# Performance work log

Measured on AMD Instinct MI355X. Metric: run time of the kernel, lower is better.

## Reference

```python
import jax, jax.numpy as jnp
import numpy as np

B, T, D_MODEL, H, RPR_K = 2, 2048, 1024, 16, 8
DK = D_MODEL // H  # 64
NUM_RPR = 2 * RPR_K + 1


def setup_inputs() -> dict:
    key = jax.random.key(0)
    ks = jax.random.split(key, 16)
    s = 0.02
    inp = {
        "query": jax.random.normal(ks[0], (B, T, D_MODEL), jnp.float32),
        "key": jax.random.normal(ks[1], (B, T, D_MODEL), jnp.float32),
        "value": jax.random.normal(ks[2], (B, T, D_MODEL), jnp.float32),
        "mask": jnp.ones((B, 1, 1, T), dtype=bool),
        "w_q": jax.random.normal(ks[3], (D_MODEL, H * DK), jnp.float32) * s,
        "b_q": jnp.zeros((H * DK,), jnp.float32),
        "w_k": jax.random.normal(ks[4], (D_MODEL, H * DK), jnp.float32) * s,
        "b_k": jnp.zeros((H * DK,), jnp.float32),
        "w_v": jax.random.normal(ks[5], (D_MODEL, H * DK), jnp.float32) * s,
        "b_v": jnp.zeros((H * DK,), jnp.float32),
        "w_o": jax.random.normal(ks[6], (H * DK, D_MODEL), jnp.float32) * s,
        "b_o": jnp.zeros((D_MODEL,), jnp.float32),
        "rpr_key_table": jax.random.normal(ks[7], (NUM_RPR, DK), jnp.float32),
        "rpr_value_table": jax.random.normal(ks[8], (NUM_RPR, DK), jnp.float32),
    }
    return inp


def _rel_edges(seq_len):
    # edges[i, j] = clamp(j - i + rpr_k, 0, 2*rpr_k)  -> [T, T] int32
    seq = jnp.arange(seq_len)
    edges = seq[None, :] - seq[:, None] + RPR_K
    return jnp.clip(edges, 0, 2 * RPR_K)


def reference(query, key, value, mask, w_q, b_q, w_k, b_k, w_v, b_v,
              w_o, b_o, rpr_key_table, rpr_value_table):
    Bsz, Tlen, _ = query.shape
    edges = _rel_edges(Tlen)                       # [T, T]
    ek = rpr_key_table[edges]                      # [T, T, DK]
    ev = rpr_value_table[edges]                    # [T, T, DK]

    def proj(x, w, b):
        return (x @ w + b).reshape(Bsz, Tlen, H, DK).transpose(0, 2, 1, 3)  # [B,H,T,DK]

    q = proj(query, w_q, b_q)
    k = proj(key, w_k, b_k)
    v = proj(value, w_v, b_v)

    scores_qk = jnp.einsum('bhtd,bhsd->bhts', q, k)
    scores_qek = jnp.einsum('bhtd,tsd->bhts', q, ek)
    scores = (scores_qk + scores_qek) / jnp.sqrt(jnp.float32(DK))
    scores = jnp.where(mask, scores, jnp.float32(-1e9))
    a = jax.nn.softmax(scores, axis=-1)            # [B,H,T,T]

    upd = jnp.einsum('bhts,bhsd->bhtd', a, v)
    upd_e = jnp.einsum('bhts,tsd->bhtd', a, ev)
    x = (upd + upd_e).transpose(0, 2, 1, 3).reshape(Bsz, Tlen, H * DK)
    return x @ w_o + b_o
```

## Files before the change

### kernel.cpp

```cpp
#include <hip/hip_runtime.h>
#include <stdint.h>


typedef unsigned short u16;
typedef __attribute__((ext_vector_type(4))) float f32x4;
typedef __attribute__((ext_vector_type(16))) float f32x16;
typedef __attribute__((ext_vector_type(4))) int   i32x4;
typedef __attribute__((ext_vector_type(8))) __bf16 bh8;

#define T_LEN 2048
#define NHEAD 16
#define NR    17

#define SCALE_LOG2 0.18033688011112042f
#define CLAMP_LOG2 86.56170245333781f

__device__ __forceinline__ float bf2f(u16 x) {
  unsigned u = ((unsigned)x) << 16;
  return __builtin_bit_cast(float, u);
}
__device__ __forceinline__ u16 f2bf(float f) {
  unsigned u = __builtin_bit_cast(unsigned, f);
  u = u + 0x7fffu + ((u >> 16) & 1u);
  return (u16)(u >> 16);
}
__device__ __forceinline__ f32x4 zero4() { f32x4 z = {0.f, 0.f, 0.f, 0.f}; return z; }
__device__ __forceinline__ f32x16 zero16() {
  f32x16 z = {0.f, 0.f, 0.f, 0.f, 0.f, 0.f, 0.f, 0.f,
              0.f, 0.f, 0.f, 0.f, 0.f, 0.f, 0.f, 0.f};
  return z;
}

__device__ __forceinline__ f32x4 mfma16(bh8 a, bh8 b, f32x4 c) {
  return __builtin_amdgcn_mfma_f32_16x16x32_bf16(a, b, c, 0, 0, 0);
}
__device__ __forceinline__ f32x16 mfma32(bh8 a, bh8 b, f32x16 c) {
  return __builtin_amdgcn_mfma_f32_32x32x16_bf16(a, b, c, 0, 0, 0);
}

__device__ __forceinline__ unsigned cvtpk(float a, float b) {
  unsigned r;
  asm("v_cvt_pk_bf16_f32 %0, %1, %2" : "=v"(r) : "v"(a), "v"(b));
  return r;
}

__device__ __forceinline__ void bar_sync() {
  __builtin_amdgcn_sched_barrier(0);
  asm volatile("s_waitcnt lgkmcnt(0)" ::: "memory");
  __builtin_amdgcn_s_barrier();
  __builtin_amdgcn_sched_barrier(0);
}

__device__ __forceinline__ void wait_vm0() {
  __builtin_amdgcn_sched_barrier(0);
  asm volatile("s_waitcnt vmcnt(0)" ::: "memory");
  __builtin_amdgcn_sched_barrier(0);
}

__device__ __forceinline__ void async16(const u16* g, u16* l) {
  __builtin_amdgcn_global_load_lds(
      (const __attribute__((address_space(1))) void*)g,
      (__attribute__((address_space(3))) void*)l, 16, 0, 0);
}

__device__ __forceinline__ bh8 ldfrag(const u16* base, int row, int qc) {
  const i32x4 v = *(const i32x4*)(base + row * 64 + ((qc ^ (row & 7)) << 3));
  return __builtin_bit_cast(bh8, v);
}

__global__ __launch_bounds__(256) void prep_kernel(
    const float* __restrict__ xq, const float* __restrict__ xk,
    const float* __restrict__ xv, const float* __restrict__ w0,
    const float* __restrict__ w1, const float* __restrict__ w2,
    const float* __restrict__ w3, u16* __restrict__ oq, u16* __restrict__ ok,
    u16* __restrict__ ov, u16* __restrict__ t0, u16* __restrict__ t1,
    u16* __restrict__ t2, u16* __restrict__ t3) {
  __shared__ u16 tile[32][33];
  const int z = blockIdx.z;
  if (z < 3) {
    const float* S = (z == 0) ? xq : (z == 1) ? xk : xv;
    u16* D = (z == 0) ? oq : (z == 1) ? ok : ov;
    const size_t i = ((size_t)blockIdx.x * 256 + threadIdx.x) * 8;
    const f32x4 v0 = *(const f32x4*)(S + i);
    const f32x4 v1 = *(const f32x4*)(S + i + 4);
    u16 o[8];
#pragma unroll
    for (int j = 0; j < 4; ++j) {
      o[j] = f2bf(v0[j]);
      o[4 + j] = f2bf(v1[j]);
    }
    i32x4 w;
    __builtin_memcpy(&w, o, 16);
    *(i32x4*)(D + i) = w;
  } else {
    if (blockIdx.x >= 1024) return;
    const float* S = (z == 3) ? w0 : (z == 4) ? w1 : (z == 5) ? w2 : w3;
    u16* D = (z == 3) ? t0 : (z == 4) ? t1 : (z == 5) ? t2 : t3;
    const int tx = threadIdx.x & 31, ty = threadIdx.x >> 5;
    const int bx = blockIdx.x & 31, by = blockIdx.x >> 5;
#pragma unroll
    for (int i = 0; i < 4; ++i) {
      const int y = by * 32 + ty + i * 8;
      tile[ty + i * 8][tx] = f2bf(S[(size_t)y * 1024 + bx * 32 + tx]);
    }
    __syncthreads();
#pragma unroll
    for (int i = 0; i < 4; ++i) {
      const int y = bx * 32 + ty + i * 8;
      D[(size_t)y * 1024 + by * 32 + tx] = tile[tx][ty + i * 8];
    }
  }
}

__device__ __forceinline__ void gemm_body(const u16* __restrict__ A,
                                          const u16* __restrict__ Bm,
                                          const float* __restrict__ bias,
                                          void* __restrict__ out, int mode,
                                          int bm, int bn) {
  __shared__ __align__(16) u16 As[2][128 * 32];
  __shared__ __align__(16) u16 Bs[2][128 * 32];
  const int tid = threadIdx.x;
  const int wv = tid >> 6;
  const int ln = tid & 63;
  const int quad = ln >> 4, l15 = ln & 15;
  const int wr = wv >> 1, wc = wv & 1;

  f32x4 acc[4][4];
#pragma unroll
  for (int i = 0; i < 4; ++i)
#pragma unroll
    for (int j = 0; j < 4; ++j) acc[i][j] = zero4();

  const int c0 = tid, c1 = tid + 256;
  const size_t aoff0 = (size_t)(bm * 128 + (c0 >> 2)) * 1024 + (c0 & 3) * 8;
  const size_t aoff1 = (size_t)(bm * 128 + (c1 >> 2)) * 1024 + (c1 & 3) * 8;
  const size_t boff0 = (size_t)(bn * 128 + (c0 >> 2)) * 1024 + (c0 & 3) * 8;
  const size_t boff1 = (size_t)(bn * 128 + (c1 >> 2)) * 1024 + (c1 & 3) * 8;

  u16* ad0[2] = {&As[0][(wv * 64) * 8], &As[1][(wv * 64) * 8]};
  u16* ad1[2] = {&As[0][(256 + wv * 64) * 8], &As[1][(256 + wv * 64) * 8]};
  u16* bd0[2] = {&Bs[0][(wv * 64) * 8], &Bs[1][(wv * 64) * 8]};
  u16* bd1[2] = {&Bs[0][(256 + wv * 64) * 8], &Bs[1][(256 + wv * 64) * 8]};

  async16(A + aoff0, ad0[0]);
  async16(A + aoff1, ad1[0]);
  async16(Bm + boff0, bd0[0]);
  async16(Bm + boff1, bd1[0]);
  __syncthreads();

  for (int kt = 0; kt < 32; ++kt) {
    const int cur = kt & 1, nxt = cur ^ 1;
    if (kt < 31) {
      const int ko = (kt + 1) * 32;
      async16(A + aoff0 + ko, ad0[nxt]);
      async16(A + aoff1 + ko, ad1[nxt]);
      async16(Bm + boff0 + ko, bd0[nxt]);
      async16(Bm + boff1 + ko, bd1[nxt]);
    }

    bh8 af[4], bf[4];
#pragma unroll
    for (int mi = 0; mi < 4; ++mi)
      af[mi] = __builtin_bit_cast(
          bh8,
          *(const i32x4*)&As[cur][(wr * 64 + mi * 16 + l15) * 32 + quad * 8]);
#pragma unroll
    for (int ni = 0; ni < 4; ++ni)
      bf[ni] = __builtin_bit_cast(
          bh8,
          *(const i32x4*)&Bs[cur][(wc * 64 + ni * 16 + l15) * 32 + quad * 8]);
#pragma unroll
    for (int mi = 0; mi < 4; ++mi)
#pragma unroll
      for (int ni = 0; ni < 4; ++ni)
        acc[mi][ni] = mfma16(af[mi], bf[ni], acc[mi][ni]);

    __syncthreads();
  }

#pragma unroll
  for (int mi = 0; mi < 4; ++mi) {
    const int row0 = bm * 128 + wr * 64 + mi * 16 + quad * 4;
#pragma unroll
    for (int ni = 0; ni < 4; ++ni) {
      const int col = bn * 128 + wc * 64 + ni * 16 + l15;
      const float bcol = (mode == 3) ? 0.f : bias[col];
#pragma unroll
      for (int reg = 0; reg < 4; ++reg) {
        const int r = row0 + reg;
        const float v = acc[mi][ni][reg] + ((mode == 3) ? bias[r] : bcol);
        if (mode == 1) {
          const int bb = r >> 11, t = r & 2047;
          const int h = col >> 6, d = col & 63;
          ((u16*)out)[(((size_t)bb * NHEAD + h) * T_LEN + (size_t)t) * 64 + d] =
              f2bf(v);
        } else {
          const int h = r >> 6, d = r & 63;
          const int bb = col >> 11, t = col & 2047;
          ((u16*)out)[(((size_t)bb * NHEAD + h) * 64 + (size_t)d) * T_LEN + t] =
              f2bf(v);
        }
      }
    }
  }
}

__global__ __launch_bounds__(256) void gemm_qkv_kernel(
    const u16* __restrict__ xq, const u16* __restrict__ xk,
    const u16* __restrict__ xv, const u16* __restrict__ wtq,
    const u16* __restrict__ wtk, const u16* __restrict__ wtv,
    const float* __restrict__ bq, const float* __restrict__ bk,
    const float* __restrict__ bv, u16* __restrict__ oq, u16* __restrict__ ok,
    u16* __restrict__ ovt) {
  const int z = blockIdx.z;
  if (z == 0)
    gemm_body(xq, wtq, bq, oq, 1, blockIdx.x, blockIdx.y);
  else if (z == 1)
    gemm_body(xk, wtk, bk, ok, 1, blockIdx.x, blockIdx.y);
  else
    gemm_body(wtv, xv, bv, ovt, 3, blockIdx.y, blockIdx.x);
}

__global__ __launch_bounds__(256) void gemm_o_kernel(const u16* __restrict__ A,
                                                     const u16* __restrict__ Bm,
                                                     const float* __restrict__ bias,
                                                     float* __restrict__ out) {
  __shared__ __align__(16) u16 As[2][64 * 32];
  __shared__ __align__(16) u16 Bs[2][128 * 32];
  const int tid = threadIdx.x;
  const int wv = tid >> 6;
  const int ln = tid & 63;
  const int quad = ln >> 4, l15 = ln & 15;
  const int wr = wv >> 1, wc = wv & 1;
  const int bm = blockIdx.x, bn = blockIdx.y;

  f32x4 acc[2][4];
#pragma unroll
  for (int i = 0; i < 2; ++i)
#pragma unroll
    for (int j = 0; j < 4; ++j) acc[i][j] = zero4();

  const int c0 = tid, c1 = tid + 256;
  const size_t aoff0 = (size_t)(bm * 64 + (c0 >> 2)) * 1024 + (c0 & 3) * 8;
  const size_t boff0 = (size_t)(bn * 128 + (c0 >> 2)) * 1024 + (c0 & 3) * 8;
  const size_t boff1 = (size_t)(bn * 128 + (c1 >> 2)) * 1024 + (c1 & 3) * 8;

  u16* ad0[2] = {&As[0][(wv * 64) * 8], &As[1][(wv * 64) * 8]};
  u16* bd0[2] = {&Bs[0][(wv * 64) * 8], &Bs[1][(wv * 64) * 8]};
  u16* bd1[2] = {&Bs[0][(256 + wv * 64) * 8], &Bs[1][(256 + wv * 64) * 8]};

  async16(A + aoff0, ad0[0]);
  async16(Bm + boff0, bd0[0]);
  async16(Bm + boff1, bd1[0]);
  __syncthreads();

  for (int kt = 0; kt < 32; ++kt) {
    const int cur = kt & 1, nxt = cur ^ 1;
    if (kt < 31) {
      const int ko = (kt + 1) * 32;
      async16(A + aoff0 + ko, ad0[nxt]);
      async16(Bm + boff0 + ko, bd0[nxt]);
      async16(Bm + boff1 + ko, bd1[nxt]);
    }

    bh8 af[2], bf[4];
#pragma unroll
    for (int mi = 0; mi < 2; ++mi)
      af[mi] = __builtin_bit_cast(
          bh8,
          *(const i32x4*)&As[cur][(wr * 32 + mi * 16 + l15) * 32 + quad * 8]);
#pragma unroll
    for (int ni = 0; ni < 4; ++ni)
      bf[ni] = __builtin_bit_cast(
          bh8,
          *(const i32x4*)&Bs[cur][(wc * 64 + ni * 16 + l15) * 32 + quad * 8]);
#pragma unroll
    for (int mi = 0; mi < 2; ++mi)
#pragma unroll
      for (int ni = 0; ni < 4; ++ni)
        acc[mi][ni] = mfma16(af[mi], bf[ni], acc[mi][ni]);

    __syncthreads();
  }

#pragma unroll
  for (int mi = 0; mi < 2; ++mi) {
    const int row0 = bm * 64 + wr * 32 + mi * 16 + quad * 4;
#pragma unroll
    for (int ni = 0; ni < 4; ++ni) {
      const int col = bn * 128 + wc * 64 + ni * 16 + l15;
      const float bcol = bias[col];
#pragma unroll
      for (int reg = 0; reg < 4; ++reg)
        out[(size_t)(row0 + reg) * 1024 + col] = acc[mi][ni][reg] + bcol;
    }
  }
}

__global__ __launch_bounds__(256, 3) void attn_kernel(
    const u16* __restrict__ Qw, const u16* __restrict__ Kw,
    const u16* __restrict__ Vtw, const float* __restrict__ rkt,
    const float* __restrict__ rvt, u16* __restrict__ U) {
  __shared__ __align__(16) u16 smu[16384];
  __shared__ float smf[4480];
  u16* const Qs = smu;
  float* const qes = smf;
  float* const aw15 = smf + 2176;
  float* const lp = smf + 4096;
  float* const aw0 = smf + 4224;
  float* const aw16 = smf + 4352;
  float* const rvs = (float*)smu;

  const int tid = threadIdx.x;
  const int wv = tid >> 6, ln = tid & 63;
  const int l31 = ln & 31, hi = ln >> 5;
  const int wg = blockIdx.x;
  const int xcd = wg & 7;
  const int slot = wg >> 3;
  const int qt = slot & 15;
  const int bh = xcd * 4 + (slot >> 4);
  const size_t hb = (size_t)bh * (T_LEN * 64);
  const int t0 = qt * 128 + wv * 32;
  const int tl = wv * 32 + l31;

  const int r8 = ln >> 3, c8 = ln & 7;
  const int kgp = c8 ^ (r8 & 7);
  const u16* ksrc0 = Kw + hb + (size_t)(wv * 16 + r8) * 64 + kgp * 8;
  const u16* ksrc1 = Kw + hb + (size_t)(wv * 16 + 8 + r8) * 64 + kgp * 8;
  const u16* vsrc0 = Vtw + hb + (size_t)(wv * 16 + r8) * T_LEN + kgp * 8;
  const u16* vsrc1 = Vtw + hb + (size_t)(wv * 16 + 8 + r8) * T_LEN + kgp * 8;
  u16* const ldsK0 = smu + (wv * 16) * 64;
  u16* const ldsK1 = smu + (wv * 16 + 8) * 64;
  u16* const ldsV0 = smu + 8192 + (wv * 16) * 64;
  u16* const ldsV1 = smu + 8192 + (wv * 16 + 8) * 64;

  {
    const u16* qsrc = Qw + hb + (size_t)(qt * 128 + wv * 32 + r8) * 64 + kgp * 8;
#pragma unroll
    for (int a = 0; a < 4; ++a)
      async16(qsrc + (size_t)(a * 8) * 64, Qs + (wv * 32 + a * 8) * 64);
  }
  wait_vm0();
  bar_sync();

  for (int i = tid; i < 128 * NR; i += 256) {
    const int row = i / NR, r = i - row * NR;
    float s = 0.f;
#pragma unroll
    for (int c = 0; c < 8; ++c) {
      const i32x4 qv = *(const i32x4*)&Qs[row * 64 + ((c ^ (row & 7)) << 3)];
      const u16* qq = (const u16*)&qv;
#pragma unroll
      for (int j = 0; j < 8; ++j) s += bf2f(qq[j]) * rkt[r * 64 + c * 8 + j];
    }
    qes[i] = s;
  }
  for (int i = tid; i < 128 * 15; i += 256) aw15[i] = 0.f;
  bar_sync();

  const float qb0 = qes[tl * NR + 0] * SCALE_LOG2;
  const float qb16 = qes[tl * NR + 16] * SCALE_LOG2;
  bh8 qf[4];
#pragma unroll
  for (int kb = 0; kb < 4; ++kb) qf[kb] = ldfrag(Qs, tl, kb * 2 + hi);
  bar_sync();

  async16(ksrc0, ldsK0);
  async16(ksrc1, ldsK1);
  async16(vsrc0, ldsV0);
  async16(vsrc1, ldsV1);
  wait_vm0();
  bar_sync();

  float l_l = 0.f, s0_l = 0.f, s16_l = 0.f;
  f32x16 oacc[2] = {zero16(), zero16()};

  for (int st = 0; st < 32; ++st) {
    const int cur = st & 1;
    const u16* Kc = smu + cur * 4096;
    const u16* Vc = smu + 8192 + cur * 4096;
    if (st < 31) {
      const int nxt = cur ^ 1;
      async16(ksrc0 + (size_t)(st + 1) * 4096, ldsK0 + nxt * 4096);
      async16(ksrc1 + (size_t)(st + 1) * 4096, ldsK1 + nxt * 4096);
      async16(vsrc0 + (size_t)(st + 1) * 64, ldsV0 + nxt * 4096);
      async16(vsrc1 + (size_t)(st + 1) * 64, ldsV1 + nxt * 4096);
    }
    __builtin_amdgcn_s_setprio(1);

#pragma unroll
    for (int sb = 0; sb < 2; ++sb) {
      f32x16 sacc = zero16();
#pragma unroll
      for (int kb = 0; kb < 4; ++kb) {
        const bh8 kf = ldfrag(Kc, sb * 32 + l31, kb * 2 + hi);
        sacc = mfma32(kf, qf[kb], sacc);
      }

      const int sbase = st * 64 + sb * 32;
      float p[16];
      if (sbase + 39 <= t0) {
        float ts = 0.f;
#pragma unroll
        for (int r = 0; r < 16; ++r) {
          const float x = fminf(sacc[r] * SCALE_LOG2 + qb0, CLAMP_LOG2);
          const float pv = __builtin_amdgcn_exp2f(x);
          p[r] = pv;
          ts += pv;
        }
        l_l += ts;
        s0_l += ts;
      } else if (sbase >= t0 + 39) {
        float ts = 0.f;
#pragma unroll
        for (int r = 0; r < 16; ++r) {
          const float x = fminf(sacc[r] * SCALE_LOG2 + qb16, CLAMP_LOG2);
          const float pv = __builtin_amdgcn_exp2f(x);
          p[r] = pv;
          ts += pv;
        }
        l_l += ts;
        s16_l += ts;
      } else {
        const int base = sbase + 4 * hi - (t0 + l31) + 8;
#pragma unroll
        for (int r = 0; r < 16; ++r) {
          int rel = base + (r & 3) + 8 * (r >> 2);
          rel = rel < 0 ? 0 : (rel > 16 ? 16 : rel);
          const float x = fminf((sacc[r] + qes[tl * NR + rel]) * SCALE_LOG2,
                                CLAMP_LOG2);
          const float pv = __builtin_amdgcn_exp2f(x);
          p[r] = pv;
          l_l += pv;
          if (rel == 0)
            s0_l += pv;
          else if (rel == 16)
            s16_l += pv;
          else
            atomicAdd(&aw15[tl * 15 + rel - 1], pv);
        }
      }

#pragma unroll
      for (int h = 0; h < 2; ++h) {
        unsigned wa = cvtpk(p[8 * h + 0], p[8 * h + 1]);
        unsigned wb = cvtpk(p[8 * h + 2], p[8 * h + 3]);
        unsigned wc = cvtpk(p[8 * h + 4], p[8 * h + 5]);
        unsigned wd = cvtpk(p[8 * h + 6], p[8 * h + 7]);
        asm("v_permlane32_swap_b32 %0, %1" : "+v"(wa), "+v"(wc));
        asm("v_permlane32_swap_b32 %0, %1" : "+v"(wb), "+v"(wd));
        const i32x4 fr = {(int)wa, (int)wb, (int)wc, (int)wd};
        const bh8 pa = __builtin_bit_cast(bh8, fr);
        const int ks = sb * 2 + h;
#pragma unroll
        for (int db = 0; db < 2; ++db) {
          const bh8 vf = ldfrag(Vc, db * 32 + l31, ks * 2 + hi);
          oacc[db] = mfma32(pa, vf, oacc[db]);
        }
      }
    }
    __builtin_amdgcn_s_setprio(0);

    wait_vm0();
    bar_sync();
  }

  l_l += __shfl_xor(l_l, 32);
  s0_l += __shfl_xor(s0_l, 32);
  s16_l += __shfl_xor(s16_l, 32);
  if (ln < 32) {
    lp[tl] = l_l;
    aw0[tl] = s0_l;
    aw16[tl] = s16_l;
  }
  for (int i = tid; i < NR * 64; i += 256) rvs[i] = rvt[i];
  __syncthreads();

  const int bb = bh >> 4, hh = bh & 15;
#pragma unroll
  for (int r = 0; r < 16; ++r) {
    const int srow = (r & 3) + 8 * (r >> 2) + 4 * hi;
    const int trow = wv * 32 + srow;
    const float linv = 1.f / lp[trow];
    float e0 = aw0[trow] * rvs[l31] + aw16[trow] * rvs[16 * 64 + l31];
    float e1 = aw0[trow] * rvs[32 + l31] + aw16[trow] * rvs[16 * 64 + 32 + l31];
#pragma unroll
    for (int rr = 1; rr < 16; ++rr) {
      const float awv = aw15[trow * 15 + rr - 1];
      e0 += awv * rvs[rr * 64 + l31];
      e1 += awv * rvs[rr * 64 + 32 + l31];
    }
    const int tg = qt * 128 + trow;
    const size_t ubase = ((size_t)bb * T_LEN + tg) * 1024 + hh * 64;
    U[ubase + l31] = f2bf((oacc[0][r] + e0) * linv);
    U[ubase + 32 + l31] = f2bf((oacc[1][r] + e1) * linv);
  }
}

extern "C" void kernel_launch(void* const* d_in, const int* in_sizes, int n_in,
                              void* d_out, int out_size, void* d_ws,
                              size_t ws_size, hipStream_t stream) {
  const float* query = (const float*)d_in[0];
  const float* key = (const float*)d_in[1];
  const float* value = (const float*)d_in[2];
  const float* w_q = (const float*)d_in[4];
  const float* b_q = (const float*)d_in[5];
  const float* w_k = (const float*)d_in[6];
  const float* b_k = (const float*)d_in[7];
  const float* w_v = (const float*)d_in[8];
  const float* b_v = (const float*)d_in[9];
  const float* w_o = (const float*)d_in[10];
  const float* b_o = (const float*)d_in[11];
  const float* rkt = (const float*)d_in[12];
  const float* rvt = (const float*)d_in[13];

  char* ws = (char*)d_ws;
  const size_t MB2 = 1u << 21, MB8 = 1u << 23;
  u16* wtq = (u16*)(ws + 0 * MB2);
  u16* wtk = (u16*)(ws + 1 * MB2);
  u16* wtv = (u16*)(ws + 2 * MB2);
  u16* wto = (u16*)(ws + 3 * MB2);
  u16* Xq = (u16*)(ws + 4 * MB2 + 0 * MB8);
  u16* Xk = (u16*)(ws + 4 * MB2 + 1 * MB8);
  u16* Xv = (u16*)(ws + 4 * MB2 + 2 * MB8);
  u16* Qw = (u16*)(ws + 4 * MB2 + 3 * MB8);
  u16* Kw = (u16*)(ws + 4 * MB2 + 4 * MB8);
  u16* Vtw = (u16*)(ws + 4 * MB2 + 5 * MB8);
  u16* Uw = (u16*)(ws + 4 * MB2 + 6 * MB8);

  prep_kernel<<<dim3(2048, 1, 7), 256, 0, stream>>>(
      query, key, value, w_q, w_k, w_v, w_o, Xq, Xk, Xv, wtq, wtk, wtv, wto);
  gemm_qkv_kernel<<<dim3(32, 8, 3), 256, 0, stream>>>(
      Xq, Xk, Xv, wtq, wtk, wtv, b_q, b_k, b_v, Qw, Kw, Vtw);
  attn_kernel<<<dim3(512), 256, 0, stream>>>(Qw, Kw, Vtw, rkt, rvt, Uw);
  gemm_o_kernel<<<dim3(64, 8), 256, 0, stream>>>(Uw, wto, b_o, (float*)d_out);
}
```

Measured before the change: 271.1 us.

## Split attention KV range across two workgroups and combine partials in new kernel

Each (batch, head, query-tile) attention job is split into two workgroups. One handles key tiles near the diagonal, where the relative-position bias varies. The other handles the far tiles, where the bias is the constant index-16 term. Partial outputs and softmax sums go to float workspace buffers, and a new combine kernel merges them, adds the rpr-value contribution and writes bf16 U in a blocked layout that the output GEMM reads. It also folds the softmax scale into the Q projection and drops the exp clamp and max-free rescaling. This doubles the workgroup count for better occupancy and load balance, at the cost of an extra kernel launch, extra fp32 traffic, and a possible overflow risk without the clamp.

```diff
diff --git a/kernel.cpp b/kernel.cpp
--- a/kernel.cpp
+++ b/kernel.cpp
@@ -13,7 +13,12 @@
 #define NR    17
 
 #define SCALE_LOG2 0.18033688011112042f
-#define CLAMP_LOG2 86.56170245333781f
+
+#define AW15_OFF 0
+#define LA_OFF   1048576
+#define A0_OFF   1114112
+#define A16_OFF  1179648
+#define LB_OFF   1245184
 
 __device__ __forceinline__ float bf2f(u16 x) {
   unsigned u = ((unsigned)x) << 16;
@@ -116,7 +121,7 @@
                                           const u16* __restrict__ Bm,
                                           const float* __restrict__ bias,
                                           void* __restrict__ out, int mode,
-                                          int bm, int bn) {
+                                          int bm, int bn, float oscale) {
   __shared__ __align__(16) u16 As[2][128 * 32];
   __shared__ __align__(16) u16 Bs[2][128 * 32];
   const int tid = threadIdx.x;
@@ -193,7 +198,7 @@
           const int bb = r >> 11, t = r & 2047;
           const int h = col >> 6, d = col & 63;
           ((u16*)out)[(((size_t)bb * NHEAD + h) * T_LEN + (size_t)t) * 64 + d] =
-              f2bf(v);
+              f2bf(v * oscale);
         } else {
           const int h = r >> 6, d = r & 63;
           const int bb = col >> 11, t = col & 2047;
@@ -214,14 +219,14 @@
     u16* __restrict__ ovt) {
   const int z = blockIdx.z;
   if (z == 0)
-    gemm_body(xq, wtq, bq, oq, 1, blockIdx.x, blockIdx.y);
+    gemm_body(xq, wtq, bq, oq, 1, blockIdx.x, blockIdx.y, SCALE_LOG2);
   else if (z == 1)
-    gemm_body(xk, wtk, bk, ok, 1, blockIdx.x, blockIdx.y);
+    gemm_body(xk, wtk, bk, ok, 1, blockIdx.x, blockIdx.y, 1.f);
   else
-    gemm_body(wtv, xv, bv, ovt, 3, blockIdx.y, blockIdx.x);
-}
-
-__global__ __launch_bounds__(256) void gemm_o_kernel(const u16* __restrict__ A,
+    gemm_body(wtv, xv, bv, ovt, 3, blockIdx.y, blockIdx.x, 1.f);
+}
+
+__global__ __launch_bounds__(256) void gemm_o_kernel(const u16* __restrict__ Ublk,
                                                      const u16* __restrict__ Bm,
                                                      const float* __restrict__ bias,
                                                      float* __restrict__ out) {
@@ -241,7 +246,9 @@
     for (int j = 0; j < 4; ++j) acc[i][j] = zero4();
 
   const int c0 = tid, c1 = tid + 256;
-  const size_t aoff0 = (size_t)(bm * 64 + (c0 >> 2)) * 1024 + (c0 & 3) * 8;
+  const int rA = bm * 64 + (c0 >> 2);
+  const int tA = rA & 2047, bbA = rA >> 11;
+  const size_t abase = (size_t)(tA >> 7);
   const size_t boff0 = (size_t)(bn * 128 + (c0 >> 2)) * 1024 + (c0 & 3) * 8;
   const size_t boff1 = (size_t)(bn * 128 + (c1 >> 2)) * 1024 + (c1 & 3) * 8;
 
@@ -249,7 +256,14 @@
   u16* bd0[2] = {&Bs[0][(wv * 64) * 8], &Bs[1][(wv * 64) * 8]};
   u16* bd1[2] = {&Bs[0][(256 + wv * 64) * 8], &Bs[1][(256 + wv * 64) * 8]};
 
-  async16(A + aoff0, ad0[0]);
+  auto aoff = [&](int kt) -> size_t {
+    const int c = kt * 32 + (c0 & 3) * 8;
+    const int h = c >> 6, d = c & 63;
+    const size_t idx = (size_t)(bbA * 16 + h) * 16 + abase;
+    return idx * 16384 + (size_t)(tA & 127) * 64 + d;
+  };
+
+  async16(Ublk + aoff(0), ad0[0]);
   async16(Bm + boff0, bd0[0]);
   async16(Bm + boff1, bd1[0]);
   __syncthreads();
@@ -258,7 +272,7 @@
     const int cur = kt & 1, nxt = cur ^ 1;
     if (kt < 31) {
       const int ko = (kt + 1) * 32;
-      async16(A + aoff0 + ko, ad0[nxt]);
+      async16(Ublk + aoff(kt + 1), ad0[nxt]);
       async16(Bm + boff0 + ko, bd0[nxt]);
       async16(Bm + boff1 + ko, bd1[nxt]);
     }
@@ -300,28 +314,43 @@
 __global__ __launch_bounds__(256, 3) void attn_kernel(
     const u16* __restrict__ Qw, const u16* __restrict__ Kw,
     const u16* __restrict__ Vtw, const float* __restrict__ rkt,
-    const float* __restrict__ rvt, u16* __restrict__ U) {
+    float* __restrict__ Oa, float* __restrict__ ObLo, float* __restrict__ ObHi,
+    float* __restrict__ awb) {
   __shared__ __align__(16) u16 smu[16384];
-  __shared__ float smf[4480];
+  __shared__ float smf[4096];
   u16* const Qs = smu;
   float* const qes = smf;
   float* const aw15 = smf + 2176;
-  float* const lp = smf + 4096;
-  float* const aw0 = smf + 4224;
-  float* const aw16 = smf + 4352;
-  float* const rvs = (float*)smu;
 
   const int tid = threadIdx.x;
   const int wv = tid >> 6, ln = tid & 63;
   const int l31 = ln & 31, hi = ln >> 5;
   const int wg = blockIdx.x;
   const int xcd = wg & 7;
-  const int slot = wg >> 3;
-  const int qt = slot & 15;
-  const int bh = xcd * 4 + (slot >> 4);
+  const int rest = wg >> 3;
+  const int sh = rest >> 6;
+  const int sub = rest & 63;
+  const int qt = sub & 15;
+  const int bh = xcd * 4 + (sub >> 4);
+  const int idx = bh * 16 + qt;
   const size_t hb = (size_t)bh * (T_LEN * 64);
   const int t0 = qt * 128 + wv * 32;
   const int tl = wv * 32 + l31;
+
+  const int cut = (2 * qt + 3 > 32) ? 32 : (2 * qt + 3);
+  const int stBeg = sh ? cut : 0;
+  const int stEnd = sh ? 32 : cut;
+
+  float* const opart = (sh == 0)
+                           ? (Oa + (size_t)idx * 8192)
+                           : (idx < 256 ? ObLo + (size_t)idx * 8192
+                                        : ObHi + (size_t)(idx - 256) * 8192);
+
+  if (stBeg >= stEnd) {
+    for (int i = tid; i < 8192; i += 256) opart[i] = 0.f;
+    if (tid < 128) awb[LB_OFF + idx * 128 + tid] = 0.f;
+    return;
+  }
 
   const int r8 = ln >> 3, c8 = ln & 7;
   const int kgp = c8 ^ (r8 & 7);
@@ -343,43 +372,61 @@
   wait_vm0();
   bar_sync();
 
-  for (int i = tid; i < 128 * NR; i += 256) {
-    const int row = i / NR, r = i - row * NR;
-    float s = 0.f;
-#pragma unroll
-    for (int c = 0; c < 8; ++c) {
-      const i32x4 qv = *(const i32x4*)&Qs[row * 64 + ((c ^ (row & 7)) << 3)];
-      const u16* qq = (const u16*)&qv;
-#pragma unroll
-      for (int j = 0; j < 8; ++j) s += bf2f(qq[j]) * rkt[r * 64 + c * 8 + j];
-    }
-    qes[i] = s;
-  }
-  for (int i = tid; i < 128 * 15; i += 256) aw15[i] = 0.f;
+  if (sh == 0) {
+    for (int i = tid; i < 128 * NR; i += 256) {
+      const int row = i / NR, r = i - row * NR;
+      float s = 0.f;
+#pragma unroll
+      for (int c = 0; c < 8; ++c) {
+        const i32x4 qv = *(const i32x4*)&Qs[row * 64 + ((c ^ (row & 7)) << 3)];
+        const u16* qq = (const u16*)&qv;
+#pragma unroll
+        for (int j = 0; j < 8; ++j) s += bf2f(qq[j]) * rkt[r * 64 + c * 8 + j];
+      }
+      qes[i] = s;
+    }
+    for (int i = tid; i < 128 * 15; i += 256) aw15[i] = 0.f;
+  } else {
+    for (int row = tid; row < 128; row += 256) {
+      float s = 0.f;
+#pragma unroll
+      for (int c = 0; c < 8; ++c) {
+        const i32x4 qv = *(const i32x4*)&Qs[row * 64 + ((c ^ (row & 7)) << 3)];
+        const u16* qq = (const u16*)&qv;
+#pragma unroll
+        for (int j = 0; j < 8; ++j)
+          s += bf2f(qq[j]) * rkt[16 * 64 + c * 8 + j];
+      }
+      qes[row * NR + 16] = s;
+    }
+  }
   bar_sync();
 
-  const float qb0 = qes[tl * NR + 0] * SCALE_LOG2;
-  const float qb16 = qes[tl * NR + 16] * SCALE_LOG2;
+  const float qb0 = (sh == 0) ? qes[tl * NR + 0] : 0.f;
+  const float qb16 = qes[tl * NR + 16];
   bh8 qf[4];
 #pragma unroll
   for (int kb = 0; kb < 4; ++kb) qf[kb] = ldfrag(Qs, tl, kb * 2 + hi);
   bar_sync();
 
-  async16(ksrc0, ldsK0);
-  async16(ksrc1, ldsK1);
-  async16(vsrc0, ldsV0);
-  async16(vsrc1, ldsV1);
+  {
+    const int b0 = stBeg & 1;
+    async16(ksrc0 + (size_t)stBeg * 4096, ldsK0 + b0 * 4096);
+    async16(ksrc1 + (size_t)stBeg * 4096, ldsK1 + b0 * 4096);
+    async16(vsrc0 + (size_t)stBeg * 64, ldsV0 + b0 * 4096);
+    async16(vsrc1 + (size_t)stBeg * 64, ldsV1 + b0 * 4096);
+  }
   wait_vm0();
   bar_sync();
 
   float l_l = 0.f, s0_l = 0.f, s16_l = 0.f;
   f32x16 oacc[2] = {zero16(), zero16()};
 
-  for (int st = 0; st < 32; ++st) {
+  for (int st = stBeg; st < stEnd; ++st) {
     const int cur = st & 1;
     const u16* Kc = smu + cur * 4096;
     const u16* Vc = smu + 8192 + cur * 4096;
-    if (st < 31) {
+    if (st + 1 < stEnd) {
       const int nxt = cur ^ 1;
       async16(ksrc0 + (size_t)(st + 1) * 4096, ldsK0 + nxt * 4096);
       async16(ksrc1 + (size_t)(st + 1) * 4096, ldsK1 + nxt * 4096);
@@ -403,8 +450,7 @@
         float ts = 0.f;
 #pragma unroll
         for (int r = 0; r < 16; ++r) {
-          const float x = fminf(sacc[r] * SCALE_LOG2 + qb0, CLAMP_LOG2);
-          const float pv = __builtin_amdgcn_exp2f(x);
+          const float pv = __builtin_amdgcn_exp2f(sacc[r] + qb0);
           p[r] = pv;
           ts += pv;
         }
@@ -414,8 +460,7 @@
         float ts = 0.f;
 #pragma unroll
         for (int r = 0; r < 16; ++r) {
-          const float x = fminf(sacc[r] * SCALE_LOG2 + qb16, CLAMP_LOG2);
-          const float pv = __builtin_amdgcn_exp2f(x);
+          const float pv = __builtin_amdgcn_exp2f(sacc[r] + qb16);
           p[r] = pv;
           ts += pv;
         }
@@ -427,9 +472,8 @@
         for (int r = 0; r < 16; ++r) {
           int rel = base + (r & 3) + 8 * (r >> 2);
           rel = rel < 0 ? 0 : (rel > 16 ? 16 : rel);
-          const float x = fminf((sacc[r] + qes[tl * NR + rel]) * SCALE_LOG2,
-                                CLAMP_LOG2);
-          const float pv = __builtin_amdgcn_exp2f(x);
+          const float pv =
+              __builtin_amdgcn_exp2f(sacc[r] + qes[tl * NR + rel]);
           p[r] = pv;
           l_l += pv;
           if (rel == 0)
@@ -468,32 +512,64 @@
   l_l += __shfl_xor(l_l, 32);
   s0_l += __shfl_xor(s0_l, 32);
   s16_l += __shfl_xor(s16_l, 32);
-  if (ln < 32) {
-    lp[tl] = l_l;
-    aw0[tl] = s0_l;
-    aw16[tl] = s16_l;
-  }
-  for (int i = tid; i < NR * 64; i += 256) rvs[i] = rvt[i];
-  __syncthreads();
-
-  const int bb = bh >> 4, hh = bh & 15;
+  if (sh == 0) {
+    if (ln < 32) {
+      awb[LA_OFF + idx * 128 + tl] = l_l;
+      awb[A0_OFF + idx * 128 + tl] = s0_l;
+      awb[A16_OFF + idx * 128 + tl] = s16_l;
+    }
+  } else {
+    if (ln < 32) awb[LB_OFF + idx * 128 + tl] = l_l;
+  }
+
 #pragma unroll
   for (int r = 0; r < 16; ++r) {
     const int srow = (r & 3) + 8 * (r >> 2) + 4 * hi;
     const int trow = wv * 32 + srow;
-    const float linv = 1.f / lp[trow];
-    float e0 = aw0[trow] * rvs[l31] + aw16[trow] * rvs[16 * 64 + l31];
-    float e1 = aw0[trow] * rvs[32 + l31] + aw16[trow] * rvs[16 * 64 + 32 + l31];
-#pragma unroll
-    for (int rr = 1; rr < 16; ++rr) {
-      const float awv = aw15[trow * 15 + rr - 1];
-      e0 += awv * rvs[rr * 64 + l31];
-      e1 += awv * rvs[rr * 64 + 32 + l31];
-    }
-    const int tg = qt * 128 + trow;
-    const size_t ubase = ((size_t)bb * T_LEN + tg) * 1024 + hh * 64;
-    U[ubase + l31] = f2bf((oacc[0][r] + e0) * linv);
-    U[ubase + 32 + l31] = f2bf((oacc[1][r] + e1) * linv);
+    opart[trow * 64 + l31] = oacc[0][r];
+    opart[trow * 64 + 32 + l31] = oacc[1][r];
+  }
+
+  if (sh == 0) {
+    __syncthreads();
+    for (int i = tid; i < 128 * 15; i += 256)
+      awb[AW15_OFF + (size_t)idx * 1920 + i] = aw15[i];
+  }
+}
+
+__global__ __launch_bounds__(256) void combine_kernel(
+    const float* __restrict__ Oa, const float* __restrict__ ObLo,
+    const float* __restrict__ ObHi, const float* __restrict__ awb,
+    const float* __restrict__ rvt, u16* __restrict__ Ublk) {
+  __shared__ float os[8192];
+  __shared__ float rvs[NR * 64];
+  const int tid = threadIdx.x;
+  const int idx = blockIdx.x;
+  const float* oa = Oa + (size_t)idx * 8192;
+  const float* ob = (idx < 256) ? ObLo + (size_t)idx * 8192
+                                : ObHi + (size_t)(idx - 256) * 8192;
+  for (int i = tid; i < 8192; i += 256) os[i] = oa[i] + ob[i];
+  for (int i = tid; i < NR * 64; i += 256) rvs[i] = rvt[i];
+  __syncthreads();
+
+  const int row = tid >> 1, d0 = (tid & 1) * 32;
+  const float lB = awb[LB_OFF + idx * 128 + row];
+  const float linv = 1.f / (awb[LA_OFF + idx * 128 + row] + lB);
+  const float a0 = awb[A0_OFF + idx * 128 + row];
+  const float a16 = awb[A16_OFF + idx * 128 + row] + lB;
+  float aw[15];
+#pragma unroll
+  for (int r = 0; r < 15; ++r)
+    aw[r] = awb[AW15_OFF + (size_t)idx * 1920 + row * 15 + r];
+
+#pragma unroll 4
+  for (int j = 0; j < 32; ++j) {
+    const int d = d0 + j;
+    float e = a0 * rvs[d] + a16 * rvs[16 * 64 + d];
+#pragma unroll
+    for (int r = 1; r < 16; ++r) e += aw[r - 1] * rvs[r * 64 + d];
+    const float u = (os[row * 64 + d] + e) * linv;
+    Ublk[(size_t)idx * 16384 + row * 64 + d] = f2bf(u);
   }
 }
 
@@ -515,23 +591,32 @@
   const float* rvt = (const float*)d_in[13];
 
   char* ws = (char*)d_ws;
-  const size_t MB2 = 1u << 21, MB8 = 1u << 23;
-  u16* wtq = (u16*)(ws + 0 * MB2);
-  u16* wtk = (u16*)(ws + 1 * MB2);
-  u16* wtv = (u16*)(ws + 2 * MB2);
-  u16* wto = (u16*)(ws + 3 * MB2);
-  u16* Xq = (u16*)(ws + 4 * MB2 + 0 * MB8);
-  u16* Xk = (u16*)(ws + 4 * MB2 + 1 * MB8);
-  u16* Xv = (u16*)(ws + 4 * MB2 + 2 * MB8);
-  u16* Qw = (u16*)(ws + 4 * MB2 + 3 * MB8);
-  u16* Kw = (u16*)(ws + 4 * MB2 + 4 * MB8);
-  u16* Vtw = (u16*)(ws + 4 * MB2 + 5 * MB8);
-  u16* Uw = (u16*)(ws + 4 * MB2 + 6 * MB8);
+  const size_t MB = 1u << 20;
+  u16* wtq = (u16*)(ws + 0 * MB);
+  u16* wtk = (u16*)(ws + 2 * MB);
+  u16* wtv = (u16*)(ws + 4 * MB);
+  u16* wto = (u16*)(ws + 6 * MB);
+  u16* Xq = (u16*)(ws + 8 * MB);
+  u16* Xk = (u16*)(ws + 16 * MB);
+  u16* Xv = (u16*)(ws + 24 * MB);
+  u16* Qw = (u16*)(ws + 32 * MB);
+  u16* Kw = (u16*)(ws + 40 * MB);
+  u16* Vtw = (u16*)(ws + 48 * MB);
+  u16* Uw = (u16*)(ws + 56 * MB);
+  float* Oa = (float*)(ws + 8 * MB);
+  float* ObLo = (float*)(ws + 24 * MB);
+  float* ObHi = (float*)(ws + 56 * MB);
+  float* awb = (float*)(ws + 0 * MB);
+  u16* Ublk = (u16*)(ws + 8 * MB);
 
   prep_kernel<<<dim3(2048, 1, 7), 256, 0, stream>>>(
       query, key, value, w_q, w_k, w_v, w_o, Xq, Xk, Xv, wtq, wtk, wtv, wto);
   gemm_qkv_kernel<<<dim3(32, 8, 3), 256, 0, stream>>>(
       Xq, Xk, Xv, wtq, wtk, wtv, b_q, b_k, b_v, Qw, Kw, Vtw);
-  attn_kernel<<<dim3(512), 256, 0, stream>>>(Qw, Kw, Vtw, rkt, rvt, Uw);
-  gemm_o_kernel<<<dim3(64, 8), 256, 0, stream>>>(Uw, wto, b_o, (float*)d_out);
-}
+  attn_kernel<<<dim3(1024), 256, 0, stream>>>(Qw, Kw, Vtw, rkt, Oa, ObLo,
+                                              ObHi, awb);
+  combine_kernel<<<dim3(512), 256, 0, stream>>>(Oa, ObLo, ObHi, awb, rvt,
+                                                Ublk);
+  gemm_o_kernel<<<dim3(64, 8), 256, 0, stream>>>(Ublk, wto, b_o,
+                                                 (float*)d_out);
+}
```

After: 282.4 us. 4.2% more time.
